# Kernel optimization log

Hardware: AMD Instinct MI355X
Metric: run time of the kernel (lower is better)

## Reference

```python
import jax, jax.numpy as jnp
import numpy as np

TOP_K = 4
B, S, H, E, F = 2, 2048, 2048, 32, 768


def setup_inputs() -> dict:
    key = jax.random.key(0)
    k0, k1, k2, k3, k4 = jax.random.split(key, 5)
    scale = 0.02
    return {
        "hidden_states": jax.random.normal(k0, (B, S, H), jnp.float32),
        "gate_w": jax.random.normal(k1, (E, H), jnp.float32) * scale,   # router Linear weight [out,in]
        "w_gate": jax.random.normal(k2, (E, H, F), jnp.float32) * scale,  # gate_proj per expert
        "w_up": jax.random.normal(k3, (E, H, F), jnp.float32) * scale,    # up_proj per expert
        "w_down": jax.random.normal(k4, (E, F, H), jnp.float32) * scale,  # down_proj per expert
    }


def reference(hidden_states, gate_w, w_gate, w_up, w_down):
    b, s, h = hidden_states.shape
    x = hidden_states.reshape(-1, h)                      # [T, H]
    T = x.shape[0]
    n_exp = gate_w.shape[0]

    # Router: logits -> float32 softmax -> top-k -> renormalize (norm_topk_prob)
    router_logits = x @ gate_w.T                          # [T, E]
    probs = jax.nn.softmax(router_logits.astype(jnp.float32), axis=-1)
    top_w, top_i = jax.lax.top_k(probs, TOP_K)            # [T, K]
    top_w = top_w / jnp.sum(top_w, axis=-1, keepdims=True)
    top_w = top_w.astype(x.dtype)

    # Dense combine matrix [T, E]: routing weight for selected experts, 0 elsewhere
    combine = jnp.zeros((T, n_exp), x.dtype).at[
        jnp.arange(T)[:, None], top_i
    ].add(top_w)

    # Scan over experts: SwiGLU MLP, weighted accumulate. Keeps peak mem ~ T*F.
    def step(acc, ws):
        wg, wu, wd, cw = ws                               # [H,F],[H,F],[F,H],[T]
        hdn = jax.nn.silu(x @ wg) * (x @ wu)              # [T, F]
        return acc + cw[:, None] * (hdn @ wd), None

    out, _ = jax.lax.scan(
        step, jnp.zeros((T, h), x.dtype), (w_gate, w_up, w_down, combine.T)
    )
    return out.reshape(b, s, h), router_logits
```

## Files before the change

kernel.cpp:

```cpp
#include <hip/hip_runtime.h>
#include <hip/hip_bf16.h>

#define T_TOK 4096
#define HID 2048
#define NE 32
#define FF 768
#define TOPK 4
#define NSLOT (T_TOK * TOPK)

typedef __bf16 bf16;
typedef __bf16 bf16x4 __attribute__((ext_vector_type(4)));
typedef __bf16 bf16x8 __attribute__((ext_vector_type(8)));
typedef float f32x4 __attribute__((ext_vector_type(4)));

__device__ __forceinline__ void async_copy16(const void* g, void* l) {
    __builtin_amdgcn_global_load_lds(
        (const __attribute__((address_space(1))) void*)g,
        (__attribute__((address_space(3))) void*)l, 16, 0, 0);
}

__global__ __launch_bounds__(256) void conv_x_kernel(
    const float* __restrict__ x, bf16* __restrict__ xb)
{
    size_t i = ((size_t)blockIdx.x * 256 + threadIdx.x) * 8;
    float4 a = *(const float4*)(x + i);
    float4 b = *(const float4*)(x + i + 4);
    bf16x8 v = {(bf16)a.x, (bf16)a.y, (bf16)a.z, (bf16)a.w,
                (bf16)b.x, (bf16)b.y, (bf16)b.z, (bf16)b.w};
    *(bf16x8*)(xb + i) = v;
}

__global__ __launch_bounds__(256) void transpose_cvt_kernel(
    const float* __restrict__ in, bf16* __restrict__ outp, int R, int C)
{
    const size_t mo = (size_t)blockIdx.z * R * C;
    const float* A = in + mo;
    bf16* O = outp + mo;
    const int c0 = blockIdx.x * 32;
    const int r0 = blockIdx.y * 64;
    __shared__ bf16 T[32][68];
    const int tid = threadIdx.x;
    const int tx = tid & 31;
    const int w = tid >> 5;
#pragma unroll
    for (int k = 0; k < 8; ++k) {
        int r = w * 8 + k;
        T[tx][r] = (bf16)A[(size_t)(r0 + r) * C + c0 + tx];
    }
    __syncthreads();
    const int c = tid >> 3;
    const int rq = tid & 7;
    bf16x4 v0 = *(const bf16x4*)&T[c][rq * 8];
    bf16x4 v1 = *(const bf16x4*)&T[c][rq * 8 + 4];
    bf16x8 v = {v0[0], v0[1], v0[2], v0[3], v1[0], v1[1], v1[2], v1[3]};
    *(bf16x8*)(O + (size_t)(c0 + c) * R + r0 + rq * 8) = v;
}

__global__ __launch_bounds__(256) void router_kernel(
    const float* __restrict__ x, const float* __restrict__ gw,
    float* __restrict__ logits_out, int* __restrict__ topi,
    float* __restrict__ topw, int* __restrict__ counts)
{
    const int t = blockIdx.x;
    __shared__ float xs[HID];
    __shared__ float lg[NE];
    __shared__ float ps[NE];
    const float4* xr = (const float4*)(x + (size_t)t * HID);
    float4* xs4 = (float4*)xs;
    for (int i = threadIdx.x; i < HID / 4; i += 256) xs4[i] = xr[i];
    __syncthreads();

    const int e = threadIdx.x >> 3;
    const int part = threadIdx.x & 7;
    const float4* gr = (const float4*)(gw + (size_t)e * HID + part * 256);
    const float4* xp = (const float4*)(xs + part * 256);
    float sum = 0.f;
#pragma unroll 8
    for (int i = 0; i < 64; ++i) {
        float4 g = gr[i], v = xp[i];
        sum += g.x * v.x + g.y * v.y + g.z * v.z + g.w * v.w;
    }
    sum += __shfl_down(sum, 4, 8);
    sum += __shfl_down(sum, 2, 8);
    sum += __shfl_down(sum, 1, 8);
    if (part == 0) { lg[e] = sum; logits_out[(size_t)t * NE + e] = sum; }
    __syncthreads();

    if (threadIdx.x == 0) {
        float mx = lg[0];
        for (int i = 1; i < NE; ++i) mx = fmaxf(mx, lg[i]);
        for (int i = 0; i < NE; ++i) ps[i] = __expf(lg[i] - mx);
        float tw[TOPK]; int ti[TOPK]; float ts = 0.f;
        for (int k = 0; k < TOPK; ++k) {
            float best = -1.f; int bi = 0;
            for (int i = 0; i < NE; ++i)
                if (ps[i] > best) { best = ps[i]; bi = i; }
            tw[k] = best; ti[k] = bi; ps[bi] = -2.f; ts += best;
        }
        const float inv = 1.f / ts;
        for (int k = 0; k < TOPK; ++k) {
            topi[t * TOPK + k] = ti[k];
            topw[t * TOPK + k] = tw[k] * inv;
            atomicAdd(&counts[ti[k]], 1);
        }
    }
}

__global__ void offsets_kernel(const int* __restrict__ counts,
                               int* __restrict__ offs, int* __restrict__ cursors)
{
    if (threadIdx.x == 0) {
        int acc = 0;
        for (int e2 = 0; e2 < NE; ++e2) { offs[e2] = acc; acc += counts[e2]; cursors[e2] = 0; }
    }
}

__global__ __launch_bounds__(256) void scatter_kernel(
    const int* __restrict__ topi, const float* __restrict__ topw,
    const int* __restrict__ offs, int* __restrict__ cursors,
    int* __restrict__ slot_token, float* __restrict__ slot_w)
{
    int t = blockIdx.x * 256 + threadIdx.x;
    if (t >= T_TOK) return;
#pragma unroll
    for (int k = 0; k < TOPK; ++k) {
        int e2 = topi[t * TOPK + k];
        int pos = atomicAdd(&cursors[e2], 1);
        int idx = offs[e2] + pos;
        slot_token[idx] = t;
        slot_w[idx] = topw[t * TOPK + k];
    }
}

__global__ __launch_bounds__(256) void gemm_gu2_kernel(
    const bf16* __restrict__ xb, const bf16* __restrict__ WT,
    const int* __restrict__ slot_token, const int* __restrict__ offs,
    const int* __restrict__ counts, bf16* __restrict__ GU, int col_off)
{
    const int nt = blockIdx.x;
    const int mt = blockIdx.y;
    const int e  = blockIdx.z;
    const int cnt = counts[e];
    if (mt * 128 >= cnt) return;
    const int off = offs[e];
    const bf16* B = WT + (size_t)e * FF * HID + (size_t)(nt * 128) * HID;

    __shared__ bf16 As[128 * 64];
    __shared__ bf16 Bs[128 * 64];
    __shared__ int toks[128];

    const int tid = threadIdx.x;
    if (tid < 128) {
        int row = mt * 128 + tid;
        toks[tid] = slot_token[off + (row < cnt ? row : cnt - 1)];
    }
    __syncthreads();

    const int srow = tid >> 3;
    const int c_lds = tid & 7;
    const bf16* aptr[4];
    const bf16* bptr[4];
#pragma unroll
    for (int q = 0; q < 4; ++q) {
        int row = q * 32 + srow;
        int cg = c_lds ^ (row & 7);
        aptr[q] = xb + (size_t)toks[row] * HID + cg * 8;
        bptr[q] = B + (size_t)row * HID + cg * 8;
    }

    const int lane = tid & 63;
    const int w  = tid >> 6;
    const int wm = (w & 1) * 64;
    const int wn = (w >> 1) * 64;
    const int fr = lane & 15;
    const int kq = lane >> 4;

    f32x4 acc[4][4];
#pragma unroll
    for (int i = 0; i < 4; ++i)
#pragma unroll
        for (int j = 0; j < 4; ++j) acc[i][j] = {0.f, 0.f, 0.f, 0.f};

    for (int kk = 0; kk < HID; kk += 64) {
        __syncthreads();
#pragma unroll
        for (int q = 0; q < 4; ++q)
            async_copy16(aptr[q] + kk, As + q * 2048 + tid * 8);
#pragma unroll
        for (int q = 0; q < 4; ++q)
            async_copy16(bptr[q] + kk, Bs + q * 2048 + tid * 8);
        __syncthreads();
#pragma unroll
        for (int ks = 0; ks < 2; ++ks) {
            bf16x8 a[4], b[4];
#pragma unroll
            for (int i = 0; i < 4; ++i) {
                int row = wm + i * 16 + fr;
                int ch = (ks * 4 + kq) ^ (row & 7);
                a[i] = *(const bf16x8*)(As + row * 64 + ch * 8);
            }
#pragma unroll
            for (int j = 0; j < 4; ++j) {
                int n = wn + j * 16 + fr;
                int ch = (ks * 4 + kq) ^ (n & 7);
                b[j] = *(const bf16x8*)(Bs + n * 64 + ch * 8);
            }
#pragma unroll
            for (int i = 0; i < 4; ++i)
#pragma unroll
                for (int j = 0; j < 4; ++j)
                    acc[i][j] = __builtin_amdgcn_mfma_f32_16x16x32_bf16(a[i], b[j], acc[i][j], 0, 0, 0);
        }
    }

    const int colBase = col_off + nt * 128 + wn;
#pragma unroll
    for (int i = 0; i < 4; ++i) {
#pragma unroll
        for (int r = 0; r < 4; ++r) {
            int mloc = wm + i * 16 + kq * 4 + r;
            int row = mt * 128 + mloc;
            if (row < cnt) {
                bf16* dst = GU + (size_t)(off + row) * (2 * FF) + colBase;
#pragma unroll
                for (int j = 0; j < 4; ++j)
                    dst[j * 16 + fr] = (bf16)acc[i][j][r];
            }
        }
    }
}

__global__ __launch_bounds__(256) void silu_mul_kernel(
    const bf16* __restrict__ GU, bf16* __restrict__ hdn)
{
    size_t idx = ((size_t)blockIdx.x * 256 + threadIdx.x) * 4;
    size_t s = idx / FF;
    int f = (int)(idx % FF);
    const bf16* gp = GU + s * (2 * FF) + f;
    bf16x4 g4 = *(const bf16x4*)gp;
    bf16x4 u4 = *(const bf16x4*)(gp + FF);
    bf16x4 o;
#pragma unroll
    for (int i = 0; i < 4; ++i) {
        float g = (float)g4[i], u = (float)u4[i];
        float sl = g / (1.f + __expf(-g));
        o[i] = (bf16)(sl * u);
    }
    *(bf16x4*)(hdn + s * FF + f) = o;
}

__global__ __launch_bounds__(256) void gemm_down2_kernel(
    const bf16* __restrict__ hdn, const bf16* __restrict__ WT,
    const int* __restrict__ slot_token, const float* __restrict__ slot_w,
    const int* __restrict__ offs, const int* __restrict__ counts,
    float* __restrict__ out)
{
    const int nt = blockIdx.x;
    const int mt = blockIdx.y;
    const int e  = blockIdx.z;
    const int cnt = counts[e];
    if (mt * 128 >= cnt) return;
    const int off = offs[e];
    const bf16* B = WT + (size_t)e * HID * FF + (size_t)(nt * 128) * FF;

    __shared__ bf16 As[128 * 64];
    __shared__ bf16 Bs[128 * 64];
    __shared__ int toks[128];
    __shared__ float wts[128];

    const int tid = threadIdx.x;
    if (tid < 128) {
        int row = mt * 128 + tid;
        if (row < cnt) { toks[tid] = slot_token[off + row]; wts[tid] = slot_w[off + row]; }
        else           { toks[tid] = 0; wts[tid] = 0.f; }
    }

    const int srow = tid >> 3;
    const int c_lds = tid & 7;
    const bf16* aptr[4];
    const bf16* bptr[4];
#pragma unroll
    for (int q = 0; q < 4; ++q) {
        int row = q * 32 + srow;
        int cg = c_lds ^ (row & 7);
        int sl = off + mt * 128 + row;
        if (sl > NSLOT - 1) sl = NSLOT - 1;
        aptr[q] = hdn + (size_t)sl * FF + cg * 8;
        bptr[q] = B + (size_t)row * FF + cg * 8;
    }

    const int lane = tid & 63;
    const int w  = tid >> 6;
    const int wm = (w & 1) * 64;
    const int wn = (w >> 1) * 64;
    const int fr = lane & 15;
    const int kq = lane >> 4;

    f32x4 acc[4][4];
#pragma unroll
    for (int i = 0; i < 4; ++i)
#pragma unroll
        for (int j = 0; j < 4; ++j) acc[i][j] = {0.f, 0.f, 0.f, 0.f};

    for (int kk = 0; kk < FF; kk += 64) {
        __syncthreads();
#pragma unroll
        for (int q = 0; q < 4; ++q)
            async_copy16(aptr[q] + kk, As + q * 2048 + tid * 8);
#pragma unroll
        for (int q = 0; q < 4; ++q)
            async_copy16(bptr[q] + kk, Bs + q * 2048 + tid * 8);
        __syncthreads();
#pragma unroll
        for (int ks = 0; ks < 2; ++ks) {
            bf16x8 a[4], b[4];
#pragma unroll
            for (int i = 0; i < 4; ++i) {
                int row = wm + i * 16 + fr;
                int ch = (ks * 4 + kq) ^ (row & 7);
                a[i] = *(const bf16x8*)(As + row * 64 + ch * 8);
            }
#pragma unroll
            for (int j = 0; j < 4; ++j) {
                int n = wn + j * 16 + fr;
                int ch = (ks * 4 + kq) ^ (n & 7);
                b[j] = *(const bf16x8*)(Bs + n * 64 + ch * 8);
            }
#pragma unroll
            for (int i = 0; i < 4; ++i)
#pragma unroll
                for (int j = 0; j < 4; ++j)
                    acc[i][j] = __builtin_amdgcn_mfma_f32_16x16x32_bf16(a[i], b[j], acc[i][j], 0, 0, 0);
        }
    }

    const int colBase = nt * 128 + wn;
#pragma unroll
    for (int i = 0; i < 4; ++i) {
#pragma unroll
        for (int r = 0; r < 4; ++r) {
            int mloc = wm + i * 16 + kq * 4 + r;
            int row = mt * 128 + mloc;
            if (row < cnt) {
                int tok = toks[mloc];
                float wgt = wts[mloc];
                float* dst = out + (size_t)tok * HID + colBase;
#pragma unroll
                for (int j = 0; j < 4; ++j)
                    atomicAdd(&dst[j * 16 + fr], acc[i][j][r] * wgt);
            }
        }
    }
}

extern "C" void kernel_launch(void* const* d_in, const int* in_sizes, int n_in,
                              void* d_out, int out_size, void* d_ws, size_t ws_size,
                              hipStream_t stream)
{
    const float* x  = (const float*)d_in[0];
    const float* gw = (const float*)d_in[1];
    const float* wg = (const float*)d_in[2];
    const float* wu = (const float*)d_in[3];
    const float* wd = (const float*)d_in[4];
    float* out    = (float*)d_out;
    float* logits = out + (size_t)T_TOK * HID;

    char* ws = (char*)d_ws;
    size_t o = 0;
    bf16* xb  = (bf16*)(ws + o); o += (size_t)T_TOK * HID * 2;
    bf16* GU  = (bf16*)(ws + o); o += (size_t)NSLOT * 1536 * 2;
    bf16* hdn = (bf16*)(ws + o); o += (size_t)NSLOT * 768 * 2;
    bf16* WT  = (bf16*)(ws + o); o += (size_t)NE * HID * FF * 2;
    int*   topi = (int*)(ws + o);        o += (size_t)T_TOK * TOPK * 4;
    float* topw = (float*)(ws + o);      o += (size_t)T_TOK * TOPK * 4;
    int*   slot_token = (int*)(ws + o);  o += (size_t)T_TOK * TOPK * 4;
    float* slot_w = (float*)(ws + o);    o += (size_t)T_TOK * TOPK * 4;
    int* counts  = (int*)(ws + o);
    int* offs    = counts + 32;
    int* cursors = counts + 64;

    hipMemsetAsync(out, 0, (size_t)T_TOK * HID * sizeof(float), stream);
    hipMemsetAsync(counts, 0, 32 * sizeof(int), stream);

    conv_x_kernel<<<(T_TOK * HID / 8) / 256, 256, 0, stream>>>(x, xb);
    router_kernel<<<T_TOK, 256, 0, stream>>>(x, gw, logits, topi, topw, counts);
    offsets_kernel<<<1, 64, 0, stream>>>(counts, offs, cursors);
    scatter_kernel<<<T_TOK / 256, 256, 0, stream>>>(topi, topw, offs, cursors, slot_token, slot_w);

    transpose_cvt_kernel<<<dim3(FF / 32, HID / 64, NE), 256, 0, stream>>>(wg, WT, HID, FF);
    gemm_gu2_kernel<<<dim3(6, 32, NE), 256, 0, stream>>>(xb, WT, slot_token, offs, counts, GU, 0);
    transpose_cvt_kernel<<<dim3(FF / 32, HID / 64, NE), 256, 0, stream>>>(wu, WT, HID, FF);
    gemm_gu2_kernel<<<dim3(6, 32, NE), 256, 0, stream>>>(xb, WT, slot_token, offs, counts, GU, FF);

    silu_mul_kernel<<<((size_t)NSLOT * 768 / 4) / 256, 256, 0, stream>>>(GU, hdn);

    transpose_cvt_kernel<<<dim3(HID / 32, FF / 64, NE), 256, 0, stream>>>(wd, WT, FF, HID);
    gemm_down2_kernel<<<dim3(16, 32, NE), 256, 0, stream>>>(hdn, WT, slot_token, slot_w, offs, counts, out);
}
```

Measured before the change: 1.103 ms.

## Double-buffer GEMM loads, fuse x conversion into router, merge gate/up GEMMs

Both expert GEMMs now double-buffer their LDS tiles: the next K-slice is prefetched asynchronously while MFMAs run on the current one, so load latency overlaps compute. The fp32-to-bf16 conversion of x moves into the router kernel, which removes one launch and one extra read of x. When the workspace is large enough, gate and up weights go to separate buffers and a single launch computes both projections. The transpose kernel switches to 64x64 tiles with vectorized loads, and silu_mul processes 8 elements per thread. In exchange, the GEMMs use twice the LDS, which can lower occupancy, and the fused path needs a larger workspace.

```diff
diff --git a/kernel.cpp b/kernel.cpp
--- a/kernel.cpp
+++ b/kernel.cpp
@@ -19,15 +19,9 @@
         (__attribute__((address_space(3))) void*)l, 16, 0, 0);
 }
 
-__global__ __launch_bounds__(256) void conv_x_kernel(
-    const float* __restrict__ x, bf16* __restrict__ xb)
-{
-    size_t i = ((size_t)blockIdx.x * 256 + threadIdx.x) * 8;
-    float4 a = *(const float4*)(x + i);
-    float4 b = *(const float4*)(x + i + 4);
-    bf16x8 v = {(bf16)a.x, (bf16)a.y, (bf16)a.z, (bf16)a.w,
-                (bf16)b.x, (bf16)b.y, (bf16)b.z, (bf16)b.w};
-    *(bf16x8*)(xb + i) = v;
+__device__ __forceinline__ void fence_barrier() {
+    __builtin_amdgcn_s_barrier();
+    asm volatile("" ::: "memory");
 }
 
 __global__ __launch_bounds__(256) void transpose_cvt_kernel(
@@ -36,30 +30,36 @@
     const size_t mo = (size_t)blockIdx.z * R * C;
     const float* A = in + mo;
     bf16* O = outp + mo;
-    const int c0 = blockIdx.x * 32;
+    const int c0 = blockIdx.x * 64;
     const int r0 = blockIdx.y * 64;
-    __shared__ bf16 T[32][68];
+    __shared__ bf16 T[64][72];
     const int tid = threadIdx.x;
-    const int tx = tid & 31;
-    const int w = tid >> 5;
-#pragma unroll
-    for (int k = 0; k < 8; ++k) {
-        int r = w * 8 + k;
-        T[tx][r] = (bf16)A[(size_t)(r0 + r) * C + c0 + tx];
+    const int rr = tid >> 4;
+    const int cc = (tid & 15) * 4;
+#pragma unroll
+    for (int p = 0; p < 4; ++p) {
+        int r = p * 16 + rr;
+        float4 v = *(const float4*)(A + (size_t)(r0 + r) * C + c0 + cc);
+        bf16x4 b = {(bf16)v.x, (bf16)v.y, (bf16)v.z, (bf16)v.w};
+        *(bf16x4*)&T[r][cc] = b;
     }
     __syncthreads();
     const int c = tid >> 3;
-    const int rq = tid & 7;
-    bf16x4 v0 = *(const bf16x4*)&T[c][rq * 8];
-    bf16x4 v1 = *(const bf16x4*)&T[c][rq * 8 + 4];
-    bf16x8 v = {v0[0], v0[1], v0[2], v0[3], v1[0], v1[1], v1[2], v1[3]};
-    *(bf16x8*)(O + (size_t)(c0 + c) * R + r0 + rq * 8) = v;
+    const int rb = (tid & 7) * 8;
+#pragma unroll
+    for (int p = 0; p < 2; ++p) {
+        int cw = p * 32 + c;
+        bf16 tmp[8] __attribute__((aligned(16)));
+#pragma unroll
+        for (int j = 0; j < 8; ++j) tmp[j] = T[rb + j][cw];
+        *(bf16x8*)(O + (size_t)(c0 + cw) * R + r0 + rb) = *(bf16x8*)tmp;
+    }
 }
 
 __global__ __launch_bounds__(256) void router_kernel(
     const float* __restrict__ x, const float* __restrict__ gw,
     float* __restrict__ logits_out, int* __restrict__ topi,
-    float* __restrict__ topw, int* __restrict__ counts)
+    float* __restrict__ topw, int* __restrict__ counts, bf16* __restrict__ xb)
 {
     const int t = blockIdx.x;
     __shared__ float xs[HID];
@@ -69,6 +69,14 @@
     float4* xs4 = (float4*)xs;
     for (int i = threadIdx.x; i < HID / 4; i += 256) xs4[i] = xr[i];
     __syncthreads();
+
+    {
+        const float4* xsp = (const float4*)xs + threadIdx.x * 2;
+        float4 a = xsp[0], b = xsp[1];
+        bf16x8 v = {(bf16)a.x, (bf16)a.y, (bf16)a.z, (bf16)a.w,
+                    (bf16)b.x, (bf16)b.y, (bf16)b.z, (bf16)b.w};
+        *(bf16x8*)(xb + (size_t)t * HID + threadIdx.x * 8) = v;
+    }
 
     const int e = threadIdx.x >> 3;
     const int part = threadIdx.x & 7;
@@ -133,20 +141,22 @@
 }
 
 __global__ __launch_bounds__(256) void gemm_gu2_kernel(
-    const bf16* __restrict__ xb, const bf16* __restrict__ WT,
+    const bf16* __restrict__ xb, const bf16* __restrict__ WTg,
+    const bf16* __restrict__ WTu,
     const int* __restrict__ slot_token, const int* __restrict__ offs,
-    const int* __restrict__ counts, bf16* __restrict__ GU, int col_off)
-{
-    const int nt = blockIdx.x;
+    const int* __restrict__ counts, bf16* __restrict__ GU, int nt_off)
+{
+    const int nt = blockIdx.x + nt_off;
     const int mt = blockIdx.y;
     const int e  = blockIdx.z;
     const int cnt = counts[e];
     if (mt * 128 >= cnt) return;
     const int off = offs[e];
-    const bf16* B = WT + (size_t)e * FF * HID + (size_t)(nt * 128) * HID;
-
-    __shared__ bf16 As[128 * 64];
-    __shared__ bf16 Bs[128 * 64];
+    const bf16* W = (nt < 6) ? WTg : WTu;
+    const bf16* B = W + (size_t)e * FF * HID + (size_t)((nt % 6) * 128) * HID;
+
+    __shared__ __attribute__((aligned(16))) bf16 As[2][8192];
+    __shared__ __attribute__((aligned(16))) bf16 Bs[2][8192];
     __shared__ int toks[128];
 
     const int tid = threadIdx.x;
@@ -181,15 +191,26 @@
 #pragma unroll
         for (int j = 0; j < 4; ++j) acc[i][j] = {0.f, 0.f, 0.f, 0.f};
 
+#pragma unroll
+    for (int q = 0; q < 4; ++q) async_copy16(aptr[q], &As[0][q * 2048 + tid * 8]);
+#pragma unroll
+    for (int q = 0; q < 4; ++q) async_copy16(bptr[q], &Bs[0][q * 2048 + tid * 8]);
+
+    int cur = 0;
     for (int kk = 0; kk < HID; kk += 64) {
-        __syncthreads();
-#pragma unroll
-        for (int q = 0; q < 4; ++q)
-            async_copy16(aptr[q] + kk, As + q * 2048 + tid * 8);
-#pragma unroll
-        for (int q = 0; q < 4; ++q)
-            async_copy16(bptr[q] + kk, Bs + q * 2048 + tid * 8);
-        __syncthreads();
+        if (kk + 64 < HID) {
+            const int nb = cur ^ 1;
+#pragma unroll
+            for (int q = 0; q < 4; ++q) async_copy16(aptr[q] + kk + 64, &As[nb][q * 2048 + tid * 8]);
+#pragma unroll
+            for (int q = 0; q < 4; ++q) async_copy16(bptr[q] + kk + 64, &Bs[nb][q * 2048 + tid * 8]);
+            asm volatile("s_waitcnt vmcnt(8)" ::: "memory");
+        } else {
+            asm volatile("s_waitcnt vmcnt(0)" ::: "memory");
+        }
+        fence_barrier();
+        const bf16* Ab = As[cur];
+        const bf16* Bb = Bs[cur];
 #pragma unroll
         for (int ks = 0; ks < 2; ++ks) {
             bf16x8 a[4], b[4];
@@ -197,13 +218,13 @@
             for (int i = 0; i < 4; ++i) {
                 int row = wm + i * 16 + fr;
                 int ch = (ks * 4 + kq) ^ (row & 7);
-                a[i] = *(const bf16x8*)(As + row * 64 + ch * 8);
+                a[i] = *(const bf16x8*)(Ab + row * 64 + ch * 8);
             }
 #pragma unroll
             for (int j = 0; j < 4; ++j) {
                 int n = wn + j * 16 + fr;
                 int ch = (ks * 4 + kq) ^ (n & 7);
-                b[j] = *(const bf16x8*)(Bs + n * 64 + ch * 8);
+                b[j] = *(const bf16x8*)(Bb + n * 64 + ch * 8);
             }
 #pragma unroll
             for (int i = 0; i < 4; ++i)
@@ -211,9 +232,12 @@
                 for (int j = 0; j < 4; ++j)
                     acc[i][j] = __builtin_amdgcn_mfma_f32_16x16x32_bf16(a[i], b[j], acc[i][j], 0, 0, 0);
         }
-    }
-
-    const int colBase = col_off + nt * 128 + wn;
+        asm volatile("s_waitcnt lgkmcnt(0)" ::: "memory");
+        fence_barrier();
+        cur ^= 1;
+    }
+
+    const int colBase = nt * 128 + wn;
 #pragma unroll
     for (int i = 0; i < 4; ++i) {
 #pragma unroll
@@ -233,20 +257,20 @@
 __global__ __launch_bounds__(256) void silu_mul_kernel(
     const bf16* __restrict__ GU, bf16* __restrict__ hdn)
 {
-    size_t idx = ((size_t)blockIdx.x * 256 + threadIdx.x) * 4;
+    size_t idx = ((size_t)blockIdx.x * 256 + threadIdx.x) * 8;
     size_t s = idx / FF;
     int f = (int)(idx % FF);
     const bf16* gp = GU + s * (2 * FF) + f;
-    bf16x4 g4 = *(const bf16x4*)gp;
-    bf16x4 u4 = *(const bf16x4*)(gp + FF);
-    bf16x4 o;
-#pragma unroll
-    for (int i = 0; i < 4; ++i) {
-        float g = (float)g4[i], u = (float)u4[i];
+    bf16x8 g8 = *(const bf16x8*)gp;
+    bf16x8 u8 = *(const bf16x8*)(gp + FF);
+    bf16x8 o;
+#pragma unroll
+    for (int i = 0; i < 8; ++i) {
+        float g = (float)g8[i], u = (float)u8[i];
         float sl = g / (1.f + __expf(-g));
         o[i] = (bf16)(sl * u);
     }
-    *(bf16x4*)(hdn + s * FF + f) = o;
+    *(bf16x8*)(hdn + s * FF + f) = o;
 }
 
 __global__ __launch_bounds__(256) void gemm_down2_kernel(
@@ -263,8 +287,8 @@
     const int off = offs[e];
     const bf16* B = WT + (size_t)e * HID * FF + (size_t)(nt * 128) * FF;
 
-    __shared__ bf16 As[128 * 64];
-    __shared__ bf16 Bs[128 * 64];
+    __shared__ __attribute__((aligned(16))) bf16 As[2][8192];
+    __shared__ __attribute__((aligned(16))) bf16 Bs[2][8192];
     __shared__ int toks[128];
     __shared__ float wts[128];
 
@@ -274,6 +298,7 @@
         if (row < cnt) { toks[tid] = slot_token[off + row]; wts[tid] = slot_w[off + row]; }
         else           { toks[tid] = 0; wts[tid] = 0.f; }
     }
+    __syncthreads();
 
     const int srow = tid >> 3;
     const int c_lds = tid & 7;
@@ -302,15 +327,26 @@
 #pragma unroll
         for (int j = 0; j < 4; ++j) acc[i][j] = {0.f, 0.f, 0.f, 0.f};
 
+#pragma unroll
+    for (int q = 0; q < 4; ++q) async_copy16(aptr[q], &As[0][q * 2048 + tid * 8]);
+#pragma unroll
+    for (int q = 0; q < 4; ++q) async_copy16(bptr[q], &Bs[0][q * 2048 + tid * 8]);
+
+    int cur = 0;
     for (int kk = 0; kk < FF; kk += 64) {
-        __syncthreads();
-#pragma unroll
-        for (int q = 0; q < 4; ++q)
-            async_copy16(aptr[q] + kk, As + q * 2048 + tid * 8);
-#pragma unroll
-        for (int q = 0; q < 4; ++q)
-            async_copy16(bptr[q] + kk, Bs + q * 2048 + tid * 8);
-        __syncthreads();
+        if (kk + 64 < FF) {
+            const int nb = cur ^ 1;
+#pragma unroll
+            for (int q = 0; q < 4; ++q) async_copy16(aptr[q] + kk + 64, &As[nb][q * 2048 + tid * 8]);
+#pragma unroll
+            for (int q = 0; q < 4; ++q) async_copy16(bptr[q] + kk + 64, &Bs[nb][q * 2048 + tid * 8]);
+            asm volatile("s_waitcnt vmcnt(8)" ::: "memory");
+        } else {
+            asm volatile("s_waitcnt vmcnt(0)" ::: "memory");
+        }
+        fence_barrier();
+        const bf16* Ab = As[cur];
+        const bf16* Bb = Bs[cur];
 #pragma unroll
         for (int ks = 0; ks < 2; ++ks) {
             bf16x8 a[4], b[4];
@@ -318,13 +354,13 @@
             for (int i = 0; i < 4; ++i) {
                 int row = wm + i * 16 + fr;
                 int ch = (ks * 4 + kq) ^ (row & 7);
-                a[i] = *(const bf16x8*)(As + row * 64 + ch * 8);
+                a[i] = *(const bf16x8*)(Ab + row * 64 + ch * 8);
             }
 #pragma unroll
             for (int j = 0; j < 4; ++j) {
                 int n = wn + j * 16 + fr;
                 int ch = (ks * 4 + kq) ^ (n & 7);
-                b[j] = *(const bf16x8*)(Bs + n * 64 + ch * 8);
+                b[j] = *(const bf16x8*)(Bb + n * 64 + ch * 8);
             }
 #pragma unroll
             for (int i = 0; i < 4; ++i)
@@ -332,6 +368,9 @@
                 for (int j = 0; j < 4; ++j)
                     acc[i][j] = __builtin_amdgcn_mfma_f32_16x16x32_bf16(a[i], b[j], acc[i][j], 0, 0, 0);
         }
+        asm volatile("s_waitcnt lgkmcnt(0)" ::: "memory");
+        fence_barrier();
+        cur ^= 1;
     }
 
     const int colBase = nt * 128 + wn;
@@ -370,7 +409,6 @@
     bf16* xb  = (bf16*)(ws + o); o += (size_t)T_TOK * HID * 2;
     bf16* GU  = (bf16*)(ws + o); o += (size_t)NSLOT * 1536 * 2;
     bf16* hdn = (bf16*)(ws + o); o += (size_t)NSLOT * 768 * 2;
-    bf16* WT  = (bf16*)(ws + o); o += (size_t)NE * HID * FF * 2;
     int*   topi = (int*)(ws + o);        o += (size_t)T_TOK * TOPK * 4;
     float* topw = (float*)(ws + o);      o += (size_t)T_TOK * TOPK * 4;
     int*   slot_token = (int*)(ws + o);  o += (size_t)T_TOK * TOPK * 4;
@@ -378,22 +416,34 @@
     int* counts  = (int*)(ws + o);
     int* offs    = counts + 32;
     int* cursors = counts + 64;
+    o += 256;
+    const size_t Welems = (size_t)NE * HID * FF;
+    bf16* WTg = (bf16*)(ws + o);
+    const bool big = ws_size >= o + 3 * Welems * sizeof(bf16);
+    bf16* WTu = big ? WTg + Welems : WTg;
+    bf16* WTd = big ? WTu + Welems : WTg;
 
     hipMemsetAsync(out, 0, (size_t)T_TOK * HID * sizeof(float), stream);
     hipMemsetAsync(counts, 0, 32 * sizeof(int), stream);
 
-    conv_x_kernel<<<(T_TOK * HID / 8) / 256, 256, 0, stream>>>(x, xb);
-    router_kernel<<<T_TOK, 256, 0, stream>>>(x, gw, logits, topi, topw, counts);
+    router_kernel<<<T_TOK, 256, 0, stream>>>(x, gw, logits, topi, topw, counts, xb);
     offsets_kernel<<<1, 64, 0, stream>>>(counts, offs, cursors);
     scatter_kernel<<<T_TOK / 256, 256, 0, stream>>>(topi, topw, offs, cursors, slot_token, slot_w);
 
-    transpose_cvt_kernel<<<dim3(FF / 32, HID / 64, NE), 256, 0, stream>>>(wg, WT, HID, FF);
-    gemm_gu2_kernel<<<dim3(6, 32, NE), 256, 0, stream>>>(xb, WT, slot_token, offs, counts, GU, 0);
-    transpose_cvt_kernel<<<dim3(FF / 32, HID / 64, NE), 256, 0, stream>>>(wu, WT, HID, FF);
-    gemm_gu2_kernel<<<dim3(6, 32, NE), 256, 0, stream>>>(xb, WT, slot_token, offs, counts, GU, FF);
-
-    silu_mul_kernel<<<((size_t)NSLOT * 768 / 4) / 256, 256, 0, stream>>>(GU, hdn);
-
-    transpose_cvt_kernel<<<dim3(HID / 32, FF / 64, NE), 256, 0, stream>>>(wd, WT, FF, HID);
-    gemm_down2_kernel<<<dim3(16, 32, NE), 256, 0, stream>>>(hdn, WT, slot_token, slot_w, offs, counts, out);
-}
+    if (big) {
+        transpose_cvt_kernel<<<dim3(FF / 64, HID / 64, NE), 256, 0, stream>>>(wg, WTg, HID, FF);
+        transpose_cvt_kernel<<<dim3(FF / 64, HID / 64, NE), 256, 0, stream>>>(wu, WTu, HID, FF);
+        transpose_cvt_kernel<<<dim3(HID / 64, FF / 64, NE), 256, 0, stream>>>(wd, WTd, FF, HID);
+        gemm_gu2_kernel<<<dim3(12, 32, NE), 256, 0, stream>>>(xb, WTg, WTu, slot_token, offs, counts, GU, 0);
+        silu_mul_kernel<<<(NSLOT * FF / 8) / 256, 256, 0, stream>>>(GU, hdn);
+        gemm_down2_kernel<<<dim3(16, 32, NE), 256, 0, stream>>>(hdn, WTd, slot_token, slot_w, offs, counts, out);
+    } else {
+        transpose_cvt_kernel<<<dim3(FF / 64, HID / 64, NE), 256, 0, stream>>>(wg, WTg, HID, FF);
+        gemm_gu2_kernel<<<dim3(6, 32, NE), 256, 0, stream>>>(xb, WTg, WTg, slot_token, offs, counts, GU, 0);
+        transpose_cvt_kernel<<<dim3(FF / 64, HID / 64, NE), 256, 0, stream>>>(wu, WTg, HID, FF);
+        gemm_gu2_kernel<<<dim3(6, 32, NE), 256, 0, stream>>>(xb, WTg, WTg, slot_token, offs, counts, GU, 6);
+        silu_mul_kernel<<<(NSLOT * FF / 8) / 256, 256, 0, stream>>>(GU, hdn);
+        transpose_cvt_kernel<<<dim3(HID / 64, FF / 64, NE), 256, 0, stream>>>(wd, WTg, FF, HID);
+        gemm_down2_kernel<<<dim3(16, 32, NE), 256, 0, stream>>>(hdn, WTg, slot_token, slot_w, offs, counts, out);
+    }
+}
```

After: 1.081 ms. 1.02x faster.
